# Performance work log

Measured on AMD Instinct MI355X. Metric: run time of the kernel, lower is better.

Reference implementation:

```python
import jax, jax.numpy as jnp
import numpy as np

# Fano-plane lines (zero-indexed imaginary units e1..e7 -> 0..6), standard octonion table:
# e1e2=e3, e1e4=e5, e1e7=e6, e2e4=e6, e2e6=e5(rev), e3e4=e7, ... encoded as cyclic triples.
_FANO = [(0, 1, 2), (0, 3, 4), (0, 6, 5), (1, 3, 5), (1, 4, 6), (2, 3, 6), (2, 5, 4)]


def _build_tables():
    mult = np.zeros((7, 7), dtype=np.int64)
    sign = np.zeros((7, 7), dtype=np.float32)
    for i, j, k in _FANO:
        mult[i, j] = k; mult[j, i] = k
        mult[j, k] = i; mult[k, j] = i
        mult[k, i] = j; mult[i, k] = j
        sign[i, j] = 1.0; sign[j, k] = 1.0; sign[k, i] = 1.0
        sign[j, i] = -1.0; sign[k, j] = -1.0; sign[i, k] = -1.0
    return mult, sign


def _cross_indices():
    mult, sign = _build_tables()
    ii, jj, kk, ss = [], [], [], []
    for i in range(7):
        for j in range(7):
            if i != j:
                ii.append(i); jj.append(j)
                kk.append(int(mult[i, j])); ss.append(float(sign[i, j]))
    return (np.array(ii, np.int32), np.array(jj, np.int32),
            np.array(kk, np.int32), np.array(ss, np.float32))


_CI, _CJ, _CK, _CS = _cross_indices()  # 42 entries each, fixed structure constants


def setup_inputs() -> dict:
    key = jax.random.key(0)
    k_a, k_b = jax.random.split(key)
    B = 4194304
    a = jax.random.normal(k_a, (B, 8), dtype=jnp.float32)
    b = jax.random.normal(k_b, (B, 8), dtype=jnp.float32)
    return {"a": a, "b": b}


def reference(a, b):
    # Cayley-Dickson: (a0 + av)(b0 + bv) = (a0 b0 - av.bv) + (a0 bv + b0 av + av x bv)
    a0, a_im = a[:, :1], a[:, 1:]  # [B,1], [B,7]
    b0, b_im = b[:, :1], b[:, 1:]
    real_part = a0 * b0 - jnp.sum(a_im * b_im, axis=-1, keepdims=True)  # [B,1]
    im_linear = a0 * b_im + b0 * a_im                                    # [B,7]
    signs = jnp.asarray(_CS, dtype=a.dtype)
    products = signs * a_im[:, _CI] * b_im[:, _CJ]                       # [B,42]
    im_cross = jnp.zeros_like(a_im).at[:, _CK].add(products)             # [B,7]
    return jnp.concatenate([real_part, im_linear + im_cross], axis=-1)   # [B,8]
```

## Files before the change

### kernel.cpp

```cpp
#include <hip/hip_runtime.h>


typedef float f32x4 __attribute__((ext_vector_type(4)));

__device__ __forceinline__ f32x4 xor1_swap(f32x4 v) {
    f32x4 r;
#pragma unroll
    for (int c = 0; c < 4; ++c)
        r[c] = __shfl_xor(v[c], 1, 64);
    return r;
}

__device__ __forceinline__ void octo_compute(f32x4 al, f32x4 ah, f32x4 bl, f32x4 bh,
                                             f32x4& ol, f32x4& oh) {
    float a0 = al[0];
    float x0 = al[1], x1 = al[2], x2 = al[3];
    float x3 = ah[0], x4 = ah[1], x5 = ah[2], x6 = ah[3];
    float b0 = bl[0];
    float y0 = bl[1], y1 = bl[2], y2 = bl[3];
    float y3 = bh[0], y4 = bh[1], y5 = bh[2], y6 = bh[3];

    float real = a0 * b0
               - (x0 * y0 + x1 * y1 + x2 * y2 + x3 * y3
                + x4 * y4 + x5 * y5 + x6 * y6);

    float c0 = x1 * y2 - x2 * y1 + x3 * y4 - x4 * y3 + x6 * y5 - x5 * y6;
    float c1 = x2 * y0 - x0 * y2 + x3 * y5 - x5 * y3 + x4 * y6 - x6 * y4;
    float c2 = x0 * y1 - x1 * y0 + x3 * y6 - x6 * y3 + x5 * y4 - x4 * y5;
    float c3 = x4 * y0 - x0 * y4 + x5 * y1 - x1 * y5 + x6 * y2 - x2 * y6;
    float c4 = x0 * y3 - x3 * y0 + x6 * y1 - x1 * y6 + x2 * y5 - x5 * y2;
    float c5 = x0 * y6 - x6 * y0 + x1 * y3 - x3 * y1 + x4 * y2 - x2 * y4;
    float c6 = x5 * y0 - x0 * y5 + x1 * y4 - x4 * y1 + x2 * y3 - x3 * y2;

    ol[0] = real;
    ol[1] = a0 * y0 + b0 * x0 + c0;
    ol[2] = a0 * y1 + b0 * x1 + c1;
    ol[3] = a0 * y2 + b0 * x2 + c2;
    oh[0] = a0 * y3 + b0 * x3 + c3;
    oh[1] = a0 * y4 + b0 * x4 + c4;
    oh[2] = a0 * y5 + b0 * x5 + c5;
    oh[3] = a0 * y6 + b0 * x6 + c6;
}

__global__ void __launch_bounds__(256)
octo_mul_coal(const f32x4* __restrict__ a4,
              const f32x4* __restrict__ b4,
              f32x4* __restrict__ o4,
              int n)
{
    const int t = threadIdx.x;
    const int tileO = blockIdx.x * 256;
    const int fb = tileO * 2;

    if (tileO + 256 <= n) {
        f32x4 ar0 = a4[fb + t];
        f32x4 ar1 = a4[fb + t + 256];
        f32x4 br0 = b4[fb + t];
        f32x4 br1 = b4[fb + t + 256];

        const bool odd = (t & 1);

        f32x4 asend = odd ? ar0 : ar1;
        f32x4 arecv = xor1_swap(asend);
        f32x4 a_h0 = odd ? arecv : ar0;
        f32x4 a_h1 = odd ? ar1 : arecv;

        f32x4 bsend = odd ? br0 : br1;
        f32x4 brecv = xor1_swap(bsend);
        f32x4 b_h0 = odd ? brecv : br0;
        f32x4 b_h1 = odd ? br1 : brecv;

        f32x4 o_h0, o_h1;
        octo_compute(a_h0, a_h1, b_h0, b_h1, o_h0, o_h1);

        f32x4 osend = odd ? o_h0 : o_h1;
        f32x4 orecv = xor1_swap(osend);
        f32x4 s_lo = odd ? orecv : o_h0;
        f32x4 s_hi = odd ? o_h1 : orecv;

        __builtin_nontemporal_store(s_lo, &o4[fb + t]);
        __builtin_nontemporal_store(s_hi, &o4[fb + t + 256]);
    } else {
        int i = tileO + t;
        if (i < n) {
            f32x4 al = a4[2 * i], ah = a4[2 * i + 1];
            f32x4 bl = b4[2 * i], bh = b4[2 * i + 1];
            f32x4 ol, oh;
            octo_compute(al, ah, bl, bh, ol, oh);
            o4[2 * i]     = ol;
            o4[2 * i + 1] = oh;
        }
    }
}

extern "C" void kernel_launch(void* const* d_in, const int* in_sizes, int n_in,
                              void* d_out, int out_size, void* d_ws, size_t ws_size,
                              hipStream_t stream) {
    const f32x4* a4 = (const f32x4*)d_in[0];
    const f32x4* b4 = (const f32x4*)d_in[1];
    f32x4* o4 = (f32x4*)d_out;
    int n = in_sizes[0] / 8;

    const int block = 256;
    int grid = (n + block - 1) / block;
    octo_mul_coal<<<grid, block, 0, stream>>>(a4, b4, o4, n);
}
```

Measured before the change: 75.27 us.

## Use persistent grid-stride blocks with register double-buffered prefetch of next tile

Replaces the one-tile-per-block launch with a fixed grid of 2048 blocks that loop over tiles in grid-stride fashion. Each iteration prefetches the next tile's a and b vectors into registers before computing and storing the current one, so loads overlap with compute and stores. The tail is handled by block 0. This doubles input register usage and cuts the number of resident waves, which could lower memory-level parallelism compared with many short-lived blocks.

```diff
diff --git a/kernel.cpp b/kernel.cpp
--- a/kernel.cpp
+++ b/kernel.cpp
@@ -42,46 +42,74 @@
     oh[3] = a0 * y6 + b0 * x6 + c6;
 }
 
+__device__ __forceinline__ void exchange_compute_store(
+    f32x4 ar0, f32x4 ar1, f32x4 br0, f32x4 br1,
+    f32x4* __restrict__ o4, int fb, int t, bool odd)
+{
+    f32x4 asend = odd ? ar0 : ar1;
+    f32x4 arecv = xor1_swap(asend);
+    f32x4 a_h0 = odd ? arecv : ar0;
+    f32x4 a_h1 = odd ? ar1 : arecv;
+
+    f32x4 bsend = odd ? br0 : br1;
+    f32x4 brecv = xor1_swap(bsend);
+    f32x4 b_h0 = odd ? brecv : br0;
+    f32x4 b_h1 = odd ? br1 : brecv;
+
+    f32x4 o_h0, o_h1;
+    octo_compute(a_h0, a_h1, b_h0, b_h1, o_h0, o_h1);
+
+    f32x4 osend = odd ? o_h0 : o_h1;
+    f32x4 orecv = xor1_swap(osend);
+    f32x4 s_lo = odd ? orecv : o_h0;
+    f32x4 s_hi = odd ? o_h1 : orecv;
+
+    __builtin_nontemporal_store(s_lo, &o4[fb + t]);
+    __builtin_nontemporal_store(s_hi, &o4[fb + t + 256]);
+}
+
 __global__ void __launch_bounds__(256)
-octo_mul_coal(const f32x4* __restrict__ a4,
+octo_mul_pipe(const f32x4* __restrict__ a4,
               const f32x4* __restrict__ b4,
               f32x4* __restrict__ o4,
               int n)
 {
     const int t = threadIdx.x;
-    const int tileO = blockIdx.x * 256;
-    const int fb = tileO * 2;
+    const bool odd = (t & 1);
+    const int nTiles = n >> 8;
+    const int stride = gridDim.x;
 
-    if (tileO + 256 <= n) {
+    int tile = blockIdx.x;
+    if (tile < nTiles) {
+        int fb = tile * 512;
         f32x4 ar0 = a4[fb + t];
         f32x4 ar1 = a4[fb + t + 256];
         f32x4 br0 = b4[fb + t];
         f32x4 br1 = b4[fb + t + 256];
 
-        const bool odd = (t & 1);
+        for (;;) {
+            int next = tile + stride;
+            bool have_next = next < nTiles;
+            f32x4 nar0, nar1, nbr0, nbr1;
+            if (have_next) {
+                int nfb = next * 512;
+                nar0 = a4[nfb + t];
+                nar1 = a4[nfb + t + 256];
+                nbr0 = b4[nfb + t];
+                nbr1 = b4[nfb + t + 256];
+            }
 
-        f32x4 asend = odd ? ar0 : ar1;
-        f32x4 arecv = xor1_swap(asend);
-        f32x4 a_h0 = odd ? arecv : ar0;
-        f32x4 a_h1 = odd ? ar1 : arecv;
+            exchange_compute_store(ar0, ar1, br0, br1, o4, fb, t, odd);
 
-        f32x4 bsend = odd ? br0 : br1;
-        f32x4 brecv = xor1_swap(bsend);
-        f32x4 b_h0 = odd ? brecv : br0;
-        f32x4 b_h1 = odd ? br1 : brecv;
+            if (!have_next) break;
+            tile = next;
+            fb = next * 512;
+            ar0 = nar0; ar1 = nar1; br0 = nbr0; br1 = nbr1;
+        }
+    }
 
-        f32x4 o_h0, o_h1;
-        octo_compute(a_h0, a_h1, b_h0, b_h1, o_h0, o_h1);
-
-        f32x4 osend = odd ? o_h0 : o_h1;
-        f32x4 orecv = xor1_swap(osend);
-        f32x4 s_lo = odd ? orecv : o_h0;
-        f32x4 s_hi = odd ? o_h1 : orecv;
-
-        __builtin_nontemporal_store(s_lo, &o4[fb + t]);
-        __builtin_nontemporal_store(s_hi, &o4[fb + t + 256]);
-    } else {
-        int i = tileO + t;
+    if (blockIdx.x == 0) {
+        int i = nTiles * 256 + t;
         if (i < n) {
             f32x4 al = a4[2 * i], ah = a4[2 * i + 1];
             f32x4 bl = b4[2 * i], bh = b4[2 * i + 1];
@@ -102,6 +130,7 @@
     int n = in_sizes[0] / 8;
 
     const int block = 256;
-    int grid = (n + block - 1) / block;
-    octo_mul_coal<<<grid, block, 0, stream>>>(a4, b4, o4, n);
+    int nTiles = n / block;
+    int grid = nTiles < 2048 ? (nTiles > 0 ? nTiles : 1) : 2048;
+    octo_mul_pipe<<<grid, block, 0, stream>>>(a4, b4, o4, n);
 }
```

Result: faster. 62.58 us (-16.9%).
